# Optimization experiments

Measured on AMD Instinct MI355X. Metric: run time of the kernel, lower is better.

## Reference

```python
import jax, jax.numpy as jnp
import numpy as np

NY, NU, NH = 64, 32, 512
NHRZ, B = 2048, 128


def setup_inputs() -> dict:
    key = jax.random.key(0)
    ks = jax.random.split(key, 8)
    # PyTorch-default-like scale: 1/sqrt(fan_in) keeps the long recurrence stable.
    s_y2x = 1.0 / np.sqrt(NY)
    s_xu2x = 1.0 / np.sqrt(NH + NU)
    s_x2y = 1.0 / np.sqrt(NH)
    return {
        "y0": jax.random.normal(ks[0], (B, NY), jnp.float32),
        "U": jax.random.normal(ks[1], (NHRZ, B, NU), jnp.float32),
        "y2x_w": jax.random.normal(ks[2], (NH, NY), jnp.float32) * s_y2x,
        "y2x_b": jax.random.normal(ks[3], (NH,), jnp.float32) * s_y2x,
        "xu2x_w": jax.random.normal(ks[4], (NH, NH + NU), jnp.float32) * s_xu2x,
        "xu2x_b": jax.random.normal(ks[5], (NH,), jnp.float32) * s_xu2x,
        "x2y_w": jax.random.normal(ks[6], (NY, NH), jnp.float32) * s_x2y,
        "x2y_b": jax.random.normal(ks[7], (NY,), jnp.float32) * s_x2y,
    }


def reference(y0, U, y2x_w, y2x_b, xu2x_w, xu2x_b, x2y_w, x2y_b):
    x0 = y0 @ y2x_w.T + y2x_b  # [B, NH]
    # x_{k+1} = A x_k + Bm u_k + b  (cat((x,u)) @ W.T == x @ A.T + u @ Bm.T)
    A = xu2x_w[:, :NH].T      # [NH, NH]
    Bm = xu2x_w[:, NH:].T     # [NU, NH]

    def step(x, u):
        xn = x @ A + u @ Bm + xu2x_b
        return xn, xn

    _, Xs = jax.lax.scan(step, x0, U)          # [NHRZ, B, NH]
    X = jnp.concatenate([x0[None], Xs], axis=0)  # [NHRZ+1, B, NH]
    Y = X @ x2y_w.T + x2y_b                      # [NHRZ+1, B, NY]
    return Y
```

## Files before the change

### kernel.cpp

```cpp
#include <hip/hip_runtime.h>


#define T_CH 64

typedef _Float16 h8 __attribute__((ext_vector_type(8)));
typedef float    f4 __attribute__((ext_vector_type(4)));

__device__ __forceinline__ f4 MFMA16(h8 a, h8 b, f4 c) {
  return __builtin_amdgcn_mfma_f32_16x16x32_f16(a, b, c, 0, 0, 0);
}
__device__ __forceinline__ int xoff(int row, int bc) {
  return row * 1024 + (bc ^ ((row & 7) << 4));
}
__device__ __forceinline__ size_t PK512(int tn, int kb, int ln) {
  return ((size_t)(tn * 64 + kb) * 16 + ln) * 8;
}

__global__ __launch_bounds__(256) void k_prep0(
    const float* __restrict__ xw, const float* __restrict__ yw,
    const float* __restrict__ xub, const float* __restrict__ y0,
    const float* __restrict__ y2xw, const float* __restrict__ y2xb,
    _Float16* __restrict__ A_pk, _Float16* __restrict__ A_rm,
    _Float16* __restrict__ SWpk, _Float16* __restrict__ R_rm,
    _Float16* __restrict__ Wst_pk, _Float16* __restrict__ x0h) {
  int tid = blockIdx.x * 256 + threadIdx.x;
  if (tid < 32768) {
    int g = tid; int ln = g & 15, kb = (g >> 4) & 63, tn = g >> 10;
    const float* s = xw + (tn * 16 + ln) * 544 + kb * 8;
    _Float16* d = A_pk + (size_t)g * 8;
#pragma unroll
    for (int j = 0; j < 8; j++) d[j] = (_Float16)s[j];
  } else if (tid < 65536) {
    int g = tid - 32768; int k = g >> 6, n8 = (g & 63) * 8;
#pragma unroll
    for (int j = 0; j < 8; j++) A_rm[(size_t)k * 512 + n8 + j] = (_Float16)xw[(size_t)(n8 + j) * 544 + k];
  } else if (tid < 69632) {
    int g = tid - 65536; int ln = g & 15, kb = (g >> 4) & 63, tn = g >> 10;
    const float* s = yw + (tn * 16 + ln) * 512 + kb * 8;
    _Float16* d = SWpk + (size_t)g * 8;
#pragma unroll
    for (int j = 0; j < 8; j++) d[j] = (_Float16)s[j];
  } else if (tid < 72704) {
    int g = tid - 69632; int row = g >> 6, n8 = (g & 63) * 8;
#pragma unroll
    for (int j = 0; j < 8; j++) {
      float v = 0.f;
      if (row < 32) v = xw[(size_t)(n8 + j) * 544 + 512 + row];
      else if (row == 32) v = xub[n8 + j];
      R_rm[(size_t)row * 512 + n8 + j] = (_Float16)v;
    }
  } else if (tid < 74752) {
    int g = tid - 72704; int ln = g & 15, gg = (g >> 4) & 3, tn = g >> 6;
    _Float16* d = Wst_pk + (size_t)g * 8;
#pragma unroll
    for (int j = 0; j < 8; j++) d[j] = (_Float16)xw[(size_t)(tn * 16 + ln) * 544 + 512 + gg * 8 + j];
  } else if (tid < 140288) {
    int id = tid - 74752;
    int bb = id >> 9, h = id & 511;
    float acc = y2xb[h];
    const float* wr = y2xw + h * 64;
    const float* yr = y0 + bb * 64;
#pragma unroll 8
    for (int i = 0; i < 64; i++) acc += yr[i] * wr[i];
    x0h[(size_t)bb * 512 + h] = (_Float16)acc;
  }
}

__global__ __launch_bounds__(256) void k_chain(
    const _Float16* __restrict__ rm_in, const _Float16* __restrict__ pk_in,
    _Float16* __restrict__ rm_out, _Float16* __restrict__ pk_out,
    _Float16* __restrict__ R_rm, _Float16* __restrict__ Wst_pk,
    _Float16* __restrict__ SWpk, int nR, int nSW, int off) {
  const int bid = blockIdx.x;
  const int tid = threadIdx.x;
  const int w = tid >> 6, ln = tid & 15, g = (tid >> 4) & 3;
  if (bid < 256) {
    const int Mb = (bid >> 4) * 32, Nb = (bid & 15) * 32;
    const int mt = w >> 1, nt = w & 1;
    const int mrow = Mb + mt * 16 + ln;
    f4 acc = {0.f, 0.f, 0.f, 0.f};
    for (int k0 = 0; k0 < 512; k0 += 32) {
      h8 af = *(const h8*)(rm_in + (size_t)mrow * 512 + k0 + g * 8);
      h8 bf = *(const h8*)(pk_in + PK512((Nb >> 4) + nt, (k0 >> 3) + g, ln));
      acc = MFMA16(af, bf, acc);
    }
    const int mr0 = Mb + mt * 16 + g * 4;
    const int n = Nb + nt * 16 + ln;
#pragma unroll
    for (int r = 0; r < 4; r++) rm_out[(size_t)(mr0 + r) * 512 + n] = (_Float16)acc[r];
    _Float16* pd = pk_out + (size_t)((n >> 4) * 64 + (mr0 >> 3)) * 128 + (n & 15) * 8 + (mr0 & 7);
#pragma unroll
    for (int r = 0; r < 4; r++) pd[r] = (_Float16)acc[r];
  } else if (bid < 256 + nR) {
    const int k = bid - 256;
    const _Float16* src = R_rm + (size_t)k * 24576;
    _Float16* dst = R_rm + (size_t)(k + off) * 24576;
    _Float16* wpk = Wst_pk + (size_t)(k + off) * 16384;
    f4 acc[3][8];
#pragma unroll
    for (int mt = 0; mt < 3; mt++)
#pragma unroll
      for (int i = 0; i < 8; i++) { f4 z = {0.f, 0.f, 0.f, 0.f}; acc[mt][i] = z; }
    for (int k0 = 0; k0 < 512; k0 += 32) {
      h8 af[3];
#pragma unroll
      for (int mt = 0; mt < 3; mt++)
        af[mt] = *(const h8*)(src + (size_t)(mt * 16 + ln) * 512 + k0 + g * 8);
#pragma unroll
      for (int i = 0; i < 8; i++) {
        h8 bf = *(const h8*)(pk_in + PK512(w * 8 + i, (k0 >> 3) + g, ln));
#pragma unroll
        for (int mt = 0; mt < 3; mt++) acc[mt][i] = MFMA16(af[mt], bf, acc[mt][i]);
      }
    }
#pragma unroll
    for (int mt = 0; mt < 3; mt++)
#pragma unroll
      for (int i = 0; i < 8; i++) {
        int tn = w * 8 + i, col = tn * 16 + ln;
        int r0 = mt * 16 + g * 4;
#pragma unroll
        for (int r = 0; r < 4; r++) dst[(size_t)(r0 + r) * 512 + col] = (_Float16)acc[mt][i][r];
        if (mt < 2) {
          _Float16* pd = wpk + ((size_t)(tn * 4 + (r0 >> 3)) * 16 + ln) * 8 + (r0 & 7);
#pragma unroll
          for (int r = 0; r < 4; r++) pd[r] = (_Float16)acc[mt][i][r];
        }
      }
  } else {
    const int q = bid - 256 - nR;
    const int t = q >> 3, mb = q & 7;
    const _Float16* src = SWpk + (size_t)t * 32768;
    _Float16* dst = SWpk + (size_t)(t + off) * 32768;
    f4 acc[4];
#pragma unroll
    for (int c = 0; c < 4; c++) { f4 z = {0.f, 0.f, 0.f, 0.f}; acc[c] = z; }
    const int rbase = mb * 64 + w * 16;
    for (int k0 = 0; k0 < 512; k0 += 32) {
      h8 af = *(const h8*)(rm_in + (size_t)(rbase + ln) * 512 + k0 + g * 8);
#pragma unroll
      for (int c = 0; c < 4; c++) {
        h8 bf = *(const h8*)(src + PK512(c, (k0 >> 3) + g, ln));
        acc[c] = MFMA16(af, bf, acc[c]);
      }
    }
    const int r0 = rbase + g * 4;
#pragma unroll
    for (int c = 0; c < 4; c++) {
      _Float16* pd = dst + ((size_t)(c * 64 + (r0 >> 3)) * 16 + ln) * 8 + (r0 & 7);
#pragma unroll
      for (int r = 0; r < 4; r++) pd[r] = (_Float16)acc[c][r];
    }
  }
}

__global__ __launch_bounds__(512) void k_aux(
    const _Float16* __restrict__ R_rm, const _Float16* __restrict__ SWpk0,
    _Float16* __restrict__ Gpk, const float* __restrict__ yw,
    const float* __restrict__ yb, float* __restrict__ ybias,
    float* __restrict__ bias32, const _Float16* __restrict__ x0h,
    float* __restrict__ Y) {
  __shared__ float gb[2048];
  const int bid = blockIdx.x;
  const int tid = threadIdx.x;
  if (bid < 32) {
    if (tid < 256) {
      const int w = tid >> 6, ln = tid & 15, g = (tid >> 4) & 3;
      const int mt = w & 1, cb = (w >> 1) * 2;
      const _Float16* src = R_rm + (size_t)bid * 24576;
      f4 acc[2];
#pragma unroll
      for (int c = 0; c < 2; c++) { f4 z = {0.f, 0.f, 0.f, 0.f}; acc[c] = z; }
      for (int k0 = 0; k0 < 512; k0 += 32) {
        h8 af = *(const h8*)(src + (size_t)(mt * 16 + ln) * 512 + k0 + g * 8);
#pragma unroll
        for (int c = 0; c < 2; c++) {
          h8 bf = *(const h8*)(SWpk0 + PK512(cb + c, (k0 >> 3) + g, ln));
          acc[c] = MFMA16(af, bf, acc[c]);
        }
      }
      const int r0 = mt * 16 + g * 4;
#pragma unroll
      for (int c = 0; c < 2; c++) {
        _Float16* pd = Gpk + (size_t)bid * 2048 + ((size_t)((cb + c) * 4 + (r0 >> 3)) * 16 + ln) * 8 + (r0 & 7);
#pragma unroll
        for (int r = 0; r < 4; r++) pd[r] = (_Float16)acc[c][r];
      }
    }
  } else if (bid == 32) {
    for (int idx = tid; idx < 2048; idx += 512) {
      int i = idx >> 6, c = idx & 63;
      const _Float16* br = R_rm + (size_t)i * 24576 + 32 * 512;
      const float* wc = yw + c * 512;
      float s = 0.f;
#pragma unroll 8
      for (int h = 0; h < 512; h++) s += (float)br[h] * wc[h];
      gb[idx] = s;
    }
    __syncthreads();
    for (int idx = tid; idx < 2048; idx += 512) {
      int t = (idx >> 6) + 1, c = idx & 63;
      float s = yb[c];
      for (int i = 0; i < t; i++) s += gb[i * 64 + c];
      ybias[t * 64 + c] = s;
    }
    for (int n = tid; n < 512; n += 512) {
      float s = 0.f;
#pragma unroll
      for (int i = 0; i < 32; i++) s += (float)R_rm[(size_t)i * 24576 + 32 * 512 + n];
      bias32[n] = s;
    }
  } else {
    const int w = tid >> 6, ln = tid & 15, g = (tid >> 4) & 3;
    f4 acc[4];
#pragma unroll
    for (int c = 0; c < 4; c++) { f4 z = {0.f, 0.f, 0.f, 0.f}; acc[c] = z; }
    for (int k0 = 0; k0 < 512; k0 += 32) {
      h8 af = *(const h8*)(x0h + (size_t)(w * 16 + ln) * 512 + k0 + g * 8);
#pragma unroll
      for (int c = 0; c < 4; c++) {
        h8 bf = *(const h8*)(SWpk0 + PK512(c, (k0 >> 3) + g, ln));
        acc[c] = MFMA16(af, bf, acc[c]);
      }
    }
#pragma unroll
    for (int c = 0; c < 4; c++) {
      int col = c * 16 + ln;
#pragma unroll
      for (int r = 0; r < 4; r++)
        Y[(size_t)(w * 16 + g * 4 + r) * 64 + col] = acc[c][r] + yb[col];
    }
  }
}

__global__ __launch_bounds__(512) void k_p1(
    const float* __restrict__ U, const _Float16* __restrict__ Wst_pk,
    const _Float16* __restrict__ x0h, const _Float16* __restrict__ A32_pk,
    const float* __restrict__ bias32, _Float16* __restrict__ Zh) {
  const int rb = blockIdx.x, j = blockIdx.y;
  const int row0 = rb * 32;
  const int tid = threadIdx.x;
  const int w = tid >> 6, ln = tid & 15, g = (tid >> 4) & 3;
  f4 acc[2][4];
#pragma unroll
  for (int tm = 0; tm < 2; tm++)
#pragma unroll
    for (int i = 0; i < 4; i++) { f4 z = {0.f, 0.f, 0.f, 0.f}; acc[tm][i] = z; }
#pragma unroll 4
  for (int t = 0; t < 32; t++) {
    const _Float16* wp = Wst_pk + (size_t)(31 - t) * 16384;
    h8 uf[2];
#pragma unroll
    for (int tm = 0; tm < 2; tm++) {
      const float* up = U + ((size_t)(j * 32 + t) * 128 + row0 + tm * 16 + ln) * 32 + g * 8;
      const float4 ua = *(const float4*)up;
      const float4 ub = *(const float4*)(up + 4);
      h8 v;
      v[0] = (_Float16)ua.x; v[1] = (_Float16)ua.y; v[2] = (_Float16)ua.z; v[3] = (_Float16)ua.w;
      v[4] = (_Float16)ub.x; v[5] = (_Float16)ub.y; v[6] = (_Float16)ub.z; v[7] = (_Float16)ub.w;
      uf[tm] = v;
    }
#pragma unroll
    for (int i = 0; i < 4; i++) {
      h8 bf = *(const h8*)(wp + ((size_t)((w * 4 + i) * 4 + g) * 16 + ln) * 8);
#pragma unroll
      for (int tm = 0; tm < 2; tm++) acc[tm][i] = MFMA16(uf[tm], bf, acc[tm][i]);
    }
  }
  if (j == 0) {
    for (int k0 = 0; k0 < 512; k0 += 32) {
      h8 af[2];
#pragma unroll
      for (int tm = 0; tm < 2; tm++)
        af[tm] = *(const h8*)(x0h + (size_t)(row0 + tm * 16 + ln) * 512 + k0 + g * 8);
#pragma unroll
      for (int i = 0; i < 4; i++) {
        h8 bf = *(const h8*)(A32_pk + PK512(w * 4 + i, (k0 >> 3) + g, ln));
#pragma unroll
        for (int tm = 0; tm < 2; tm++) acc[tm][i] = MFMA16(af[tm], bf, acc[tm][i]);
      }
    }
  }
#pragma unroll
  for (int tm = 0; tm < 2; tm++)
#pragma unroll
    for (int i = 0; i < 4; i++) {
      const int n = (w * 4 + i) * 16 + ln;
      const float bz = bias32[n];
#pragma unroll
      for (int r = 0; r < 4; r++) {
        const int mr = tm * 16 + g * 4 + r;
        Zh[((size_t)j * 128 + row0 + mr) * 512 + n] = (_Float16)(acc[tm][i][r] + bz);
      }
    }
}

__global__ __launch_bounds__(512) void k_scan(
    const _Float16* __restrict__ Zin, _Float16* __restrict__ Zout,
    const _Float16* __restrict__ P_pk, int d) {
  extern __shared__ char smem[];
  const int rb = blockIdx.x, j = blockIdx.y;
  const int row0 = rb * 16;
  const int tid = threadIdx.x;
  if (j < d) {
    const uint4* s = (const uint4*)(Zin + ((size_t)j * 128 + row0) * 512);
    uint4* dst = (uint4*)(Zout + ((size_t)j * 128 + row0) * 512);
#pragma unroll
    for (int q = 0; q < 2; q++) dst[tid + q * 512] = s[tid + q * 512];
    return;
  }
  const int w = tid >> 6, ln = tid & 15, g = (tid >> 4) & 3;
  {
    const int row = tid >> 5;
    const int c = (tid & 31) * 16;
    const _Float16* s = Zin + ((size_t)(j - d) * 128 + row0 + row) * 512 + c;
#pragma unroll
    for (int q = 0; q < 2; q++)
      *(h8*)(smem + xoff(row, 2 * (c + q * 8))) = *(const h8*)(s + q * 8);
  }
  __syncthreads();
  f4 acc[4];
#pragma unroll
  for (int i = 0; i < 4; i++) {
    const int n = (w * 4 + i) * 16 + ln;
#pragma unroll
    for (int r = 0; r < 4; r++)
      acc[i][r] = (float)Zin[((size_t)j * 128 + row0 + g * 4 + r) * 512 + n];
  }
#pragma unroll 4
  for (int k0 = 0; k0 < 512; k0 += 32) {
    h8 xa = *(const h8*)(smem + xoff(ln, 2 * k0 + 16 * g));
#pragma unroll
    for (int i = 0; i < 4; i++) {
      h8 bf = *(const h8*)(P_pk + PK512(w * 4 + i, (k0 >> 3) + g, ln));
      acc[i] = MFMA16(xa, bf, acc[i]);
    }
  }
#pragma unroll
  for (int i = 0; i < 4; i++) {
    const int n = (w * 4 + i) * 16 + ln;
#pragma unroll
    for (int r = 0; r < 4; r++)
      Zout[((size_t)j * 128 + row0 + g * 4 + r) * 512 + n] = (_Float16)acc[i][r];
  }
}

__global__ __launch_bounds__(512) void k_p2(
    const float* __restrict__ U, const _Float16* __restrict__ Zh,
    const _Float16* __restrict__ x0h, const _Float16* __restrict__ SWpk,
    const _Float16* __restrict__ Gpk, const float* __restrict__ ybias,
    float* __restrict__ Y) {
  const int b = blockIdx.x;
  const int r = b >> 3;
  const int j = (b & 7) * 8 + (r >> 4);
  const int ta = (r & 15) + 1, tb = 33 - ta;
  const int tid = threadIdx.x;
  const int w = tid >> 6, ln = tid & 15, g = (tid >> 4) & 3;
  const int row = w * 16 + ln;
  const _Float16* S = (j == 0) ? x0h : (Zh + (size_t)(j - 1) * 65536);
  const _Float16* SWa = SWpk + (size_t)ta * 32768;
  const _Float16* SWb = SWpk + (size_t)tb * 32768;
  f4 acc[2][4];
#pragma unroll
  for (int th = 0; th < 2; th++)
#pragma unroll
    for (int c = 0; c < 4; c++) { f4 z = {0.f, 0.f, 0.f, 0.f}; acc[th][c] = z; }
#pragma unroll 4
  for (int k0 = 0; k0 < 512; k0 += 32) {
    h8 af = *(const h8*)(S + (size_t)row * 512 + k0 + g * 8);
#pragma unroll
    for (int c = 0; c < 4; c++) {
      h8 b0 = *(const h8*)(SWa + PK512(c, (k0 >> 3) + g, ln));
      acc[0][c] = MFMA16(af, b0, acc[0][c]);
      h8 b1 = *(const h8*)(SWb + PK512(c, (k0 >> 3) + g, ln));
      acc[1][c] = MFMA16(af, b1, acc[1][c]);
    }
  }
  const size_t ubase = ((size_t)(j * 32) * 128 + row) * 32 + g * 8;
#pragma unroll 2
  for (int i = 0; i < ta; ++i) {
    const float* up = U + ubase + (size_t)i * 4096;
    const float4 ua = *(const float4*)up;
    const float4 ub = *(const float4*)(up + 4);
    h8 af;
    af[0] = (_Float16)ua.x; af[1] = (_Float16)ua.y; af[2] = (_Float16)ua.z; af[3] = (_Float16)ua.w;
    af[4] = (_Float16)ub.x; af[5] = (_Float16)ub.y; af[6] = (_Float16)ub.z; af[7] = (_Float16)ub.w;
    const _Float16* ga = Gpk + (size_t)(ta - 1 - i) * 2048;
    const _Float16* gbp = Gpk + (size_t)(tb - 1 - i) * 2048;
#pragma unroll
    for (int c = 0; c < 4; c++) {
      acc[0][c] = MFMA16(af, *(const h8*)(ga + ((size_t)(c * 4 + g) * 16 + ln) * 8), acc[0][c]);
      acc[1][c] = MFMA16(af, *(const h8*)(gbp + ((size_t)(c * 4 + g) * 16 + ln) * 8), acc[1][c]);
    }
  }
#pragma unroll 2
  for (int i = ta; i < tb; ++i) {
    const float* up = U + ubase + (size_t)i * 4096;
    const float4 ua = *(const float4*)up;
    const float4 ub = *(const float4*)(up + 4);
    h8 af;
    af[0] = (_Float16)ua.x; af[1] = (_Float16)ua.y; af[2] = (_Float16)ua.z; af[3] = (_Float16)ua.w;
    af[4] = (_Float16)ub.x; af[5] = (_Float16)ub.y; af[6] = (_Float16)ub.z; af[7] = (_Float16)ub.w;
    const _Float16* gbp = Gpk + (size_t)(tb - 1 - i) * 2048;
#pragma unroll
    for (int c = 0; c < 4; c++)
      acc[1][c] = MFMA16(af, *(const h8*)(gbp + ((size_t)(c * 4 + g) * 16 + ln) * 8), acc[1][c]);
  }
#pragma unroll
  for (int th = 0; th < 2; th++) {
    const int tw = th ? tb : ta;
    const size_t ybase = (size_t)(j * 32 + tw) * 128;
#pragma unroll
    for (int c = 0; c < 4; c++) {
      const int col = c * 16 + ln;
      const float yv = ybias[tw * 64 + col];
#pragma unroll
      for (int rr = 0; rr < 4; rr++)
        Y[(ybase + w * 16 + g * 4 + rr) * 64 + col] = acc[th][c][rr] + yv;
    }
  }
}

extern "C" void kernel_launch(void* const* d_in, const int* in_sizes, int n_in,
                              void* d_out, int out_size, void* d_ws, size_t ws_size,
                              hipStream_t stream) {
  const float* y0   = (const float*)d_in[0];
  const float* U    = (const float*)d_in[1];
  const float* y2xw = (const float*)d_in[2];
  const float* y2xb = (const float*)d_in[3];
  const float* xw   = (const float*)d_in[4];
  const float* xub  = (const float*)d_in[5];
  const float* x2yw = (const float*)d_in[6];
  const float* x2yb = (const float*)d_in[7];
  float* Y = (float*)d_out;
  char* ws = (char*)d_ws;

  _Float16* A_rm  = (_Float16*)(ws + 0x000000);
  _Float16* A_pk  = (_Float16*)(ws + 0x080000);
  auto rm = [&](int m) { return (_Float16*)(ws + 0x100000 + (size_t)(m - 1) * 0x80000); };
  auto pkL = [&](int m) { return (_Float16*)(ws + 0x480000 + (size_t)(m - 1) * 0x80000); };
  _Float16* R_rm  = (_Float16*)(ws + 0x680000);
  _Float16* Z2    = (_Float16*)(ws + 0x000000);
  _Float16* Zh    = (_Float16*)(ws + 0x800000);
  auto pkH = [&](int m) { return (_Float16*)(ws + 0x1000000 + (size_t)(m - 5) * 0x80000); };
  _Float16* Wst_pk = (_Float16*)(ws + 0x1200000);
  _Float16* SWpk   = (_Float16*)(ws + 0x1300000);
  _Float16* Gpk    = (_Float16*)(ws + 0x1510000);
  float*    ybias  = (float*)   (ws + 0x1530000);
  float*    bias32 = (float*)   (ws + 0x1534000);
  _Float16* x0h    = (_Float16*)(ws + 0x1538000);
  auto pw_rm = [&](int m) { return m == 0 ? A_rm : rm(m); };
  auto pw_pk = [&](int m) { return m == 0 ? A_pk : (m <= 4 ? pkL(m) : pkH(m)); };

  k_prep0<<<548, 256, 0, stream>>>(xw, x2yw, xub, y0, y2xw, y2xb,
                                   A_pk, A_rm, SWpk, R_rm, Wst_pk, x0h);
  for (int m = 0; m < 8; m++) {
    int nR = (m <= 4) ? (1 << m) : 0;
    int nSW = (m <= 4) ? (1 << m) : (m == 5 ? 1 : 0);
    int off = (m == 5) ? 32 : (1 << m);
    _Float16* rmo = (m == 7) ? rm(1) : rm(m + 1);
    k_chain<<<256 + nR + 8 * nSW, 256, 0, stream>>>(
        pw_rm(m), pw_pk(m), rmo, pw_pk(m + 1), R_rm, Wst_pk, SWpk, nR, nSW, off);
  }
  k_aux<<<34, 512, 0, stream>>>(R_rm, SWpk, Gpk, x2yw, x2yb, ybias, bias32, x0h, Y);
  k_p1<<<dim3(4, T_CH), 512, 0, stream>>>(U, Wst_pk, x0h, pkH(5), bias32, Zh);
  k_scan<<<dim3(8, T_CH), 512, 16384, stream>>>(Zh, Z2, pkH(5), 1);
  k_scan<<<dim3(8, T_CH), 512, 16384, stream>>>(Z2, Zh, pkH(6), 2);
  k_scan<<<dim3(8, T_CH), 512, 16384, stream>>>(Zh, Z2, pkH(7), 4);
  k_scan<<<dim3(8, T_CH), 512, 16384, stream>>>(Z2, Zh, pkH(8), 8);
  k_p2<<<1024, 512, 0, stream>>>(U, Zh, x0h, SWpk, Gpk, ybias, Y);
}
```

Before: 608.4 us.

## Restructure k_p2 to stage state and U fragments in LDS across split waves

k_p2 now splits each block's work by batch half (64 rows) and assigns waves to (time-offset, column tile) pairs instead of rows. The 64x512 state slice is staged once into swizzled shared memory, and U fragments are converted to fp16 in groups of four timesteps into a shared buffer reused by all waves. The grid is doubled to 2048 blocks. This cuts redundant global loads of state and U per wave and lets each wave reuse one B fragment across four M tiles. The cost is 80KB of LDS per block, which may limit occupancy, plus extra barriers in the U loop.

```diff
diff --git a/kernel.cpp b/kernel.cpp
--- a/kernel.cpp
+++ b/kernel.cpp
@@ -350,75 +350,88 @@
     const _Float16* __restrict__ x0h, const _Float16* __restrict__ SWpk,
     const _Float16* __restrict__ Gpk, const float* __restrict__ ybias,
     float* __restrict__ Y) {
-  const int b = blockIdx.x;
-  const int r = b >> 3;
-  const int j = (b & 7) * 8 + (r >> 4);
-  const int ta = (r & 15) + 1, tb = 33 - ta;
-  const int tid = threadIdx.x;
-  const int w = tid >> 6, ln = tid & 15, g = (tid >> 4) & 3;
-  const int row = w * 16 + ln;
+  __shared__ char Ssw[65536];
+  __shared__ char Ufr[16384];
+  const int b = blockIdx.x, tid = threadIdx.x;
+  const int lb = b >> 3;
+  const int j = (b & 7) * 8 + (lb >> 5);
+  const int q = lb & 31;
+  const int h = q >> 4, p = q & 15;
+  const int ta = p + 1, tb = 33 - ta;
+  const int row0 = h * 64;
+  const int w = tid >> 6, ln = tid & 15, g = (tid >> 4) & 3, l = tid & 63;
+  const int th = w >> 2, c = w & 3;
+  const int t_th = th ? tb : ta;
   const _Float16* S = (j == 0) ? x0h : (Zh + (size_t)(j - 1) * 65536);
-  const _Float16* SWa = SWpk + (size_t)ta * 32768;
-  const _Float16* SWb = SWpk + (size_t)tb * 32768;
-  f4 acc[2][4];
-#pragma unroll
-  for (int th = 0; th < 2; th++)
-#pragma unroll
-    for (int c = 0; c < 4; c++) { f4 z = {0.f, 0.f, 0.f, 0.f}; acc[th][c] = z; }
+
+  auto stageU = [&](int ph) {
+#pragma unroll
+    for (int fo = 0; fo < 2; fo++) {
+      const int fi = tid + fo * 512;
+      const int i4 = fi >> 8, mt = (fi >> 6) & 3, fl = fi & 63;
+      const int fln = fl & 15, fg = fl >> 4;
+      const float* up = U + ((size_t)(j * 32 + ph * 4 + i4) * 128 + row0 + mt * 16 + fln) * 32 + fg * 8;
+      const float4 ua = *(const float4*)up;
+      const float4 ub = *(const float4*)(up + 4);
+      h8 v;
+      v[0] = (_Float16)ua.x; v[1] = (_Float16)ua.y; v[2] = (_Float16)ua.z; v[3] = (_Float16)ua.w;
+      v[4] = (_Float16)ub.x; v[5] = (_Float16)ub.y; v[6] = (_Float16)ub.z; v[7] = (_Float16)ub.w;
+      *(h8*)(Ufr + (size_t)fi * 16) = v;
+    }
+  };
+
+  {
+    const int row = tid >> 3;
+    const int c0 = (tid & 7) * 64;
+    const _Float16* sp = S + (size_t)(row0 + row) * 512 + c0;
+#pragma unroll
+    for (int qq = 0; qq < 8; qq++)
+      *(h8*)(Ssw + xoff(row, 2 * (c0 + qq * 8))) = *(const h8*)(sp + qq * 8);
+  }
+  stageU(0);
+  __syncthreads();
+
+  f4 acc[4];
+#pragma unroll
+  for (int mt = 0; mt < 4; mt++) { f4 z = {0.f, 0.f, 0.f, 0.f}; acc[mt] = z; }
+  const _Float16* SW = SWpk + (size_t)t_th * 32768;
 #pragma unroll 4
   for (int k0 = 0; k0 < 512; k0 += 32) {
-    h8 af = *(const h8*)(S + (size_t)row * 512 + k0 + g * 8);
-#pragma unroll
-    for (int c = 0; c < 4; c++) {
-      h8 b0 = *(const h8*)(SWa + PK512(c, (k0 >> 3) + g, ln));
-      acc[0][c] = MFMA16(af, b0, acc[0][c]);
-      h8 b1 = *(const h8*)(SWb + PK512(c, (k0 >> 3) + g, ln));
-      acc[1][c] = MFMA16(af, b1, acc[1][c]);
-    }
-  }
-  const size_t ubase = ((size_t)(j * 32) * 128 + row) * 32 + g * 8;
-#pragma unroll 2
-  for (int i = 0; i < ta; ++i) {
-    const float* up = U + ubase + (size_t)i * 4096;
-    const float4 ua = *(const float4*)up;
-    const float4 ub = *(const float4*)(up + 4);
-    h8 af;
-    af[0] = (_Float16)ua.x; af[1] = (_Float16)ua.y; af[2] = (_Float16)ua.z; af[3] = (_Float16)ua.w;
-    af[4] = (_Float16)ub.x; af[5] = (_Float16)ub.y; af[6] = (_Float16)ub.z; af[7] = (_Float16)ub.w;
-    const _Float16* ga = Gpk + (size_t)(ta - 1 - i) * 2048;
-    const _Float16* gbp = Gpk + (size_t)(tb - 1 - i) * 2048;
-#pragma unroll
-    for (int c = 0; c < 4; c++) {
-      acc[0][c] = MFMA16(af, *(const h8*)(ga + ((size_t)(c * 4 + g) * 16 + ln) * 8), acc[0][c]);
-      acc[1][c] = MFMA16(af, *(const h8*)(gbp + ((size_t)(c * 4 + g) * 16 + ln) * 8), acc[1][c]);
-    }
-  }
-#pragma unroll 2
-  for (int i = ta; i < tb; ++i) {
-    const float* up = U + ubase + (size_t)i * 4096;
-    const float4 ua = *(const float4*)up;
-    const float4 ub = *(const float4*)(up + 4);
-    h8 af;
-    af[0] = (_Float16)ua.x; af[1] = (_Float16)ua.y; af[2] = (_Float16)ua.z; af[3] = (_Float16)ua.w;
-    af[4] = (_Float16)ub.x; af[5] = (_Float16)ub.y; af[6] = (_Float16)ub.z; af[7] = (_Float16)ub.w;
-    const _Float16* gbp = Gpk + (size_t)(tb - 1 - i) * 2048;
-#pragma unroll
-    for (int c = 0; c < 4; c++)
-      acc[1][c] = MFMA16(af, *(const h8*)(gbp + ((size_t)(c * 4 + g) * 16 + ln) * 8), acc[1][c]);
-  }
-#pragma unroll
-  for (int th = 0; th < 2; th++) {
-    const int tw = th ? tb : ta;
-    const size_t ybase = (size_t)(j * 32 + tw) * 128;
-#pragma unroll
-    for (int c = 0; c < 4; c++) {
-      const int col = c * 16 + ln;
-      const float yv = ybias[tw * 64 + col];
-#pragma unroll
-      for (int rr = 0; rr < 4; rr++)
-        Y[(ybase + w * 16 + g * 4 + rr) * 64 + col] = acc[th][c][rr] + yv;
-    }
-  }
+    h8 bf = *(const h8*)(SW + PK512(c, (k0 >> 3) + g, ln));
+#pragma unroll
+    for (int mt = 0; mt < 4; mt++) {
+      h8 af = *(const h8*)(Ssw + xoff(mt * 16 + ln, 2 * k0 + 16 * g));
+      acc[mt] = MFMA16(af, bf, acc[mt]);
+    }
+  }
+  const int nph = (tb + 3) >> 2;
+  for (int ph = 0; ph < nph; ph++) {
+#pragma unroll
+    for (int i4 = 0; i4 < 4; i4++) {
+      const int i = ph * 4 + i4;
+      if (i < t_th) {
+        h8 bf = *(const h8*)(Gpk + (size_t)(t_th - 1 - i) * 2048 + ((size_t)(c * 4 + g) * 16 + ln) * 8);
+#pragma unroll
+        for (int mt = 0; mt < 4; mt++) {
+          h8 af = *(const h8*)(Ufr + (size_t)((i4 * 4 + mt) * 64 + l) * 16);
+          acc[mt] = MFMA16(af, bf, acc[mt]);
+        }
+      }
+    }
+    if (ph + 1 < nph) {
+      __syncthreads();
+      stageU(ph + 1);
+      __syncthreads();
+    }
+  }
+  const size_t ybase = (size_t)(j * 32 + t_th) * 128;
+  const int col = c * 16 + ln;
+  const float yv = ybias[t_th * 64 + col];
+#pragma unroll
+  for (int mt = 0; mt < 4; mt++)
+#pragma unroll
+    for (int r = 0; r < 4; r++)
+      Y[(ybase + row0 + mt * 16 + g * 4 + r) * 64 + col] = acc[mt][r] + yv;
 }
 
 extern "C" void kernel_launch(void* const* d_in, const int* in_sizes, int n_in,
@@ -468,5 +481,5 @@
   k_scan<<<dim3(8, T_CH), 512, 16384, stream>>>(Z2, Zh, pkH(6), 2);
   k_scan<<<dim3(8, T_CH), 512, 16384, stream>>>(Zh, Z2, pkH(7), 4);
   k_scan<<<dim3(8, T_CH), 512, 16384, stream>>>(Z2, Zh, pkH(8), 8);
-  k_p2<<<1024, 512, 0, stream>>>(U, Zh, x0h, SWpk, Gpk, ybias, Y);
-}
+  k_p2<<<2048, 512, 0, stream>>>(U, Zh, x0h, SWpk, Gpk, ybias, Y);
+}
```

New measurement: 570.5 us. -6.2%, faster.
